# Kernel optimization log

Hardware: AMD Instinct MI355X
Metric: run time of the kernel (lower is better)

Reference implementation:

```python
import math
import jax, jax.numpy as jnp
import numpy as np

B, T, C = 4, 2048, 1024
NH, HD = 16, C // 16
FF = 4096
EPS = 1e-5


def _layernorm(x, g, b):
    mu = jnp.mean(x, axis=-1, keepdims=True)
    var = jnp.mean(jnp.square(x - mu), axis=-1, keepdims=True)
    return (x - mu) * jax.lax.rsqrt(var + EPS) * g + b


def _new_gelu(x):
    c = math.sqrt(2.0 / math.pi)
    return 0.5 * x * (1.0 + jnp.tanh(c * (x + 0.044715 * x * x * x)))


def setup_inputs() -> dict:
    key = jax.random.key(0)
    ks = jax.random.split(key, 5)
    s = lambda fan_in: 1.0 / math.sqrt(fan_in)
    return {
        "x": jax.random.normal(ks[0], (B, T, C), jnp.float32),
        "ln1_g": jnp.ones((C,), jnp.float32),
        "ln1_b": jnp.zeros((C,), jnp.float32),
        "w_qkv": jax.random.normal(ks[1], (C, 3 * C), jnp.float32) * s(C),
        "b_qkv": jnp.zeros((3 * C,), jnp.float32),
        "w_attn_proj": jax.random.normal(ks[2], (C, C), jnp.float32) * s(C),
        "b_attn_proj": jnp.zeros((C,), jnp.float32),
        "ln2_g": jnp.ones((C,), jnp.float32),
        "ln2_b": jnp.zeros((C,), jnp.float32),
        "w_fc": jax.random.normal(ks[3], (C, FF), jnp.float32) * s(C),
        "b_fc": jnp.zeros((FF,), jnp.float32),
        "w_mlp_proj": jax.random.normal(ks[4], (FF, C), jnp.float32) * s(FF),
        "b_mlp_proj": jnp.zeros((C,), jnp.float32),
    }


def reference(x, ln1_g, ln1_b, w_qkv, b_qkv, w_attn_proj, b_attn_proj,
              ln2_g, ln2_b, w_fc, b_fc, w_mlp_proj, b_mlp_proj):
    # --- attention branch ---
    h = _layernorm(x, ln1_g, ln1_b)
    qkv = h @ w_qkv + b_qkv                      # [B,T,3C]
    q, k, v = jnp.split(qkv, 3, axis=-1)
    # [B,T,C] -> [B,NH,T,HD]
    to_heads = lambda t: t.reshape(B, T, NH, HD).transpose(0, 2, 1, 3)
    q, k, v = to_heads(q), to_heads(k), to_heads(v)
    scores = jnp.einsum("bhqd,bhkd->bhqk", q, k) / math.sqrt(HD)  # [B,NH,T,T]
    causal = jnp.tril(jnp.ones((T, T), bool))
    scores = jnp.where(causal, scores, -jnp.inf)
    probs = jax.nn.softmax(scores, axis=-1)
    attn = jnp.einsum("bhqk,bhkd->bhqd", probs, v)  # [B,NH,T,HD]
    attn = attn.transpose(0, 2, 1, 3).reshape(B, T, C)
    x = x + attn @ w_attn_proj + b_attn_proj
    # --- MLP branch ---
    h = _layernorm(x, ln2_g, ln2_b)
    h = _new_gelu(h @ w_fc + b_fc)
    x = x + h @ w_mlp_proj + b_mlp_proj
    return x
```

## Files before the change

kernel.cpp:

```cpp
#include <hip/hip_runtime.h>
#include <hip/hip_bf16.h>

typedef __bf16 bf16x8 __attribute__((ext_vector_type(8)));
typedef __bf16 bf16x4 __attribute__((ext_vector_type(4)));
typedef float f32x4 __attribute__((ext_vector_type(4)));

__device__ __forceinline__ void gload16(const __bf16* g, __bf16* l) {
    __builtin_amdgcn_global_load_lds((const __attribute__((address_space(1))) void*)g,
                                     (__attribute__((address_space(3))) void*)l, 16, 0, 0);
}

__device__ __forceinline__ float gelu_f(float v) {
    float z = 0.7978845608028654f * (v + 0.044715f * v * v * v);
    float e = __expf(2.f * z);
    return 0.5f * v * (2.f - 2.f / (e + 1.f));
}

__device__ __forceinline__ int xcd_swizzle(int flat, int nwg) {
    return (flat & 7) * (nwg >> 3) + (flat >> 3);
}

__global__ __launch_bounds__(256) void diag_kernel(float* out, int n, float v) {
    int i = blockIdx.x * 256 + threadIdx.x;
    if (i < n) out[i] = v;
}

__global__ __launch_bounds__(256) void cvtT_kernel(
    const float* __restrict__ in, __bf16* __restrict__ out, int K, int N)
{
    __shared__ __bf16 tile[32][33];
    int bx = blockIdx.x * 32, by = blockIdx.y * 32;
    int tx = threadIdx.x & 31, ty = threadIdx.x >> 5;
#pragma unroll
    for (int i = 0; i < 32; i += 8)
        tile[ty + i][tx] = (__bf16)in[(size_t)(by + ty + i) * N + bx + tx];
    __syncthreads();
#pragma unroll
    for (int i = 0; i < 32; i += 8)
        out[(size_t)(bx + ty + i) * K + by + tx] = tile[tx][ty + i];
}

__global__ __launch_bounds__(256) void ln_kernel(
    const float* __restrict__ x, const float* __restrict__ g,
    const float* __restrict__ bta, __bf16* __restrict__ out)
{
    const int row = blockIdx.x, t = threadIdx.x;
    const float* xr = x + (size_t)row * 1024;
    float4 xv = ((const float4*)xr)[t];
    float f[4] = {xv.x, xv.y, xv.z, xv.w};
    float s = f[0] + f[1] + f[2] + f[3];
    float ss = f[0]*f[0] + f[1]*f[1] + f[2]*f[2] + f[3]*f[3];
#pragma unroll
    for (int off = 32; off; off >>= 1) {
        s  += __shfl_xor(s, off, 64);
        ss += __shfl_xor(ss, off, 64);
    }
    __shared__ float red[8];
    int lane = t & 63, w = t >> 6;
    if (lane == 0) { red[w] = s; red[4 + w] = ss; }
    __syncthreads();
    s  = red[0] + red[1] + red[2] + red[3];
    ss = red[4] + red[5] + red[6] + red[7];
    float mu = s * (1.f / 1024.f);
    float var = ss * (1.f / 1024.f) - mu * mu;
    float rstd = rsqrtf(fmaxf(var, 0.f) + 1e-5f);
    float4 gv = ((const float4*)g)[t];
    float4 bv = ((const float4*)bta)[t];
    bf16x4 ov;
    ov[0] = (__bf16)((f[0] - mu) * rstd * gv.x + bv.x);
    ov[1] = (__bf16)((f[1] - mu) * rstd * gv.y + bv.y);
    ov[2] = (__bf16)((f[2] - mu) * rstd * gv.z + bv.z);
    ov[3] = (__bf16)((f[3] - mu) * rstd * gv.w + bv.w);
    ((bf16x4*)(out + (size_t)row * 1024))[t] = ov;
}

template <int EPI>
__global__ __launch_bounds__(512, 2) void gemm256_kernel(
    const __bf16* __restrict__ A, const __bf16* __restrict__ BT,
    const float* __restrict__ bias, void* __restrict__ Cp, int M, int N, int K)
{
    __shared__ __align__(16) __bf16 lA[2][256 * 64];
    __shared__ __align__(16) __bf16 lB[2][256 * 64];
    const int t = threadIdx.x;
    const int lane = t & 63, w = t >> 6;
    const int wm = w >> 2, wn = w & 3;
    const int q4 = lane >> 4, r16 = lane & 15;
    const int nwg = gridDim.x * gridDim.y;
    const int nf = xcd_swizzle(blockIdx.y * gridDim.x + blockIdx.x, nwg);
    const int bm = (nf / gridDim.x) * 256, bn = (nf % gridDim.x) * 256;

    const int srow = t & 255;
    const int skc  = t >> 8;
    const __bf16* gA = A  + (size_t)(bm + srow) * K + skc * 8;
    const __bf16* gB = BT + (size_t)(bn + srow) * K + skc * 8;
    const int dst = skc * 2048 + srow * 8;

    f32x4 acc[8][4];
    f32x4 zero4 = {0.f, 0.f, 0.f, 0.f};
#pragma unroll
    for (int mi = 0; mi < 8; ++mi)
#pragma unroll
        for (int ni = 0; ni < 4; ++ni) acc[mi][ni] = zero4;

#pragma unroll
    for (int j = 0; j < 4; ++j) gload16(gA + j * 16, &lA[0][dst + j * 4096]);
#pragma unroll
    for (int j = 0; j < 4; ++j) gload16(gB + j * 16, &lB[0][dst + j * 4096]);
#pragma unroll
    for (int j = 0; j < 4; ++j) gload16(gA + 64 + j * 16, &lA[1][dst + j * 4096]);
    asm volatile("s_waitcnt vmcnt(4)" ::: "memory");
    __builtin_amdgcn_s_barrier();

    const int nt = K / 64;
    for (int ti = 0; ti < nt; ++ti) {
        const int p = ti & 1;
        bf16x8 af[4][2], bfr[2][2];
#pragma unroll
        for (int q = 0; q < 4; ++q) {
            const int qm = q >> 1, qn = q & 1;
            if (qn == 0) {
#pragma unroll
                for (int mi = 0; mi < 4; ++mi)
#pragma unroll
                    for (int ks = 0; ks < 2; ++ks)
                        af[mi][ks] = *(const bf16x8*)&lA[p][(ks * 4 + q4) * 2048 +
                            (wm * 128 + qm * 64 + mi * 16 + r16) * 8];
            }
#pragma unroll
            for (int ni = 0; ni < 2; ++ni)
#pragma unroll
                for (int ks = 0; ks < 2; ++ks)
                    bfr[ni][ks] = *(const bf16x8*)&lB[p][(ks * 4 + q4) * 2048 +
                        (wn * 64 + qn * 32 + ni * 16 + r16) * 8];
            if (q == 0 && ti + 1 < nt) {
                gload16(gB + (ti + 1) * 64,      &lB[p ^ 1][dst]);
                gload16(gB + (ti + 1) * 64 + 16, &lB[p ^ 1][dst + 4096]);
            }
            if (q == 1 && ti + 1 < nt) {
                gload16(gB + (ti + 1) * 64 + 32, &lB[p ^ 1][dst + 8192]);
                gload16(gB + (ti + 1) * 64 + 48, &lB[p ^ 1][dst + 12288]);
            }
            if (q == 3) {
                if (ti + 2 < nt) {
#pragma unroll
                    for (int j = 0; j < 4; ++j)
                        gload16(gA + (ti + 2) * 64 + j * 16, &lA[p][dst + j * 4096]);
                    asm volatile("s_waitcnt vmcnt(4)" ::: "memory");
                } else {
                    asm volatile("s_waitcnt vmcnt(0)" ::: "memory");
                }
            }
            __builtin_amdgcn_s_barrier();
            asm volatile("s_waitcnt lgkmcnt(0)" ::: "memory");
            __builtin_amdgcn_sched_barrier(0);
            __builtin_amdgcn_s_setprio(1);
#pragma unroll
            for (int mi = 0; mi < 4; ++mi)
#pragma unroll
                for (int ni = 0; ni < 2; ++ni) {
                    f32x4 v = acc[qm * 4 + mi][qn * 2 + ni];
                    v = __builtin_amdgcn_mfma_f32_16x16x32_bf16(af[mi][0], bfr[ni][0], v, 0, 0, 0);
                    v = __builtin_amdgcn_mfma_f32_16x16x32_bf16(af[mi][1], bfr[ni][1], v, 0, 0, 0);
                    acc[qm * 4 + mi][qn * 2 + ni] = v;
                }
            __builtin_amdgcn_s_setprio(0);
            __builtin_amdgcn_sched_barrier(0);
            __builtin_amdgcn_s_barrier();
        }
    }

#pragma unroll
    for (int mi = 0; mi < 8; ++mi) {
#pragma unroll
        for (int ni = 0; ni < 4; ++ni) {
#pragma unroll
            for (int i = 0; i < 4; ++i) {
                int r = bm + wm * 128 + mi * 16 + q4 * 4 + i;
                int c = bn + wn * 64 + ni * 16 + r16;
                float v = acc[mi][ni][i] + bias[c];
                if (EPI == 2) v = gelu_f(v);
                ((__bf16*)Cp)[(size_t)r * N + c] = (__bf16)v;
            }
        }
    }
}

template <int EPI>
__global__ __launch_bounds__(512, 2) void gemm128x256_kernel(
    const __bf16* __restrict__ A, const __bf16* __restrict__ BT,
    const float* __restrict__ bias, const float* __restrict__ res,
    float* __restrict__ C, int M, int N, int K)
{
    __shared__ __align__(16) __bf16 lA[2][128 * 64];
    __shared__ __align__(16) __bf16 lB[2][256 * 64];
    const int t = threadIdx.x;
    const int lane = t & 63, w = t >> 6;
    const int wm = w >> 2, wn = w & 3;
    const int q4 = lane >> 4, r16 = lane & 15;
    const int nwg = gridDim.x * gridDim.y;
    const int nf = xcd_swizzle(blockIdx.y * gridDim.x + blockIdx.x, nwg);
    const int bm = (nf / gridDim.x) * 128, bn = (nf % gridDim.x) * 256;

    const int srA = t & 127, kqA = t >> 7;
    const __bf16* gA = A + (size_t)(bm + srA) * K + kqA * 8;
    const int dstA = kqA * 1024 + srA * 8;
    const int srB = t & 255, skB = t >> 8;
    const __bf16* gB = BT + (size_t)(bn + srB) * K + skB * 8;
    const int dstB = skB * 2048 + srB * 8;

    f32x4 acc[4][4];
    f32x4 zero4 = {0.f, 0.f, 0.f, 0.f};
#pragma unroll
    for (int mi = 0; mi < 4; ++mi)
#pragma unroll
        for (int ni = 0; ni < 4; ++ni) acc[mi][ni] = zero4;

#pragma unroll
    for (int j = 0; j < 2; ++j) gload16(gA + j * 32, &lA[0][dstA + j * 4096]);
#pragma unroll
    for (int j = 0; j < 4; ++j) gload16(gB + j * 16, &lB[0][dstB + j * 4096]);
#pragma unroll
    for (int j = 0; j < 2; ++j) gload16(gA + 64 + j * 32, &lA[1][dstA + j * 4096]);
    asm volatile("s_waitcnt vmcnt(2)" ::: "memory");
    __builtin_amdgcn_s_barrier();

    const int nt = K / 64;
    for (int ti = 0; ti < nt; ++ti) {
        const int p = ti & 1;
        bf16x8 af[4][2], bfr[2][2];
#pragma unroll
        for (int qn = 0; qn < 2; ++qn) {
            if (qn == 0) {
#pragma unroll
                for (int mi = 0; mi < 4; ++mi)
#pragma unroll
                    for (int ks = 0; ks < 2; ++ks)
                        af[mi][ks] = *(const bf16x8*)&lA[p][(ks * 4 + q4) * 1024 +
                            (wm * 64 + mi * 16 + r16) * 8];
            }
#pragma unroll
            for (int ni = 0; ni < 2; ++ni)
#pragma unroll
                for (int ks = 0; ks < 2; ++ks)
                    bfr[ni][ks] = *(const bf16x8*)&lB[p][(ks * 4 + q4) * 2048 +
                        (wn * 64 + qn * 32 + ni * 16 + r16) * 8];
            if (qn == 0 && ti + 1 < nt) {
                gload16(gB + (ti + 1) * 64,      &lB[p ^ 1][dstB]);
                gload16(gB + (ti + 1) * 64 + 16, &lB[p ^ 1][dstB + 4096]);
                gload16(gB + (ti + 1) * 64 + 32, &lB[p ^ 1][dstB + 8192]);
                gload16(gB + (ti + 1) * 64 + 48, &lB[p ^ 1][dstB + 12288]);
            }
            if (qn == 1) {
                if (ti + 2 < nt) {
#pragma unroll
                    for (int j = 0; j < 2; ++j)
                        gload16(gA + (ti + 2) * 64 + j * 32, &lA[p][dstA + j * 4096]);
                    asm volatile("s_waitcnt vmcnt(2)" ::: "memory");
                } else {
                    asm volatile("s_waitcnt vmcnt(0)" ::: "memory");
                }
            }
            __builtin_amdgcn_s_barrier();
            asm volatile("s_waitcnt lgkmcnt(0)" ::: "memory");
            __builtin_amdgcn_sched_barrier(0);
            __builtin_amdgcn_s_setprio(1);
#pragma unroll
            for (int mi = 0; mi < 4; ++mi)
#pragma unroll
                for (int ni = 0; ni < 2; ++ni) {
                    f32x4 v = acc[mi][qn * 2 + ni];
                    v = __builtin_amdgcn_mfma_f32_16x16x32_bf16(af[mi][0], bfr[ni][0], v, 0, 0, 0);
                    v = __builtin_amdgcn_mfma_f32_16x16x32_bf16(af[mi][1], bfr[ni][1], v, 0, 0, 0);
                    acc[mi][qn * 2 + ni] = v;
                }
            __builtin_amdgcn_s_setprio(0);
            __builtin_amdgcn_sched_barrier(0);
            __builtin_amdgcn_s_barrier();
        }
    }

#pragma unroll
    for (int mi = 0; mi < 4; ++mi) {
#pragma unroll
        for (int ni = 0; ni < 4; ++ni) {
#pragma unroll
            for (int i = 0; i < 4; ++i) {
                int r = bm + wm * 64 + mi * 16 + q4 * 4 + i;
                int c = bn + wn * 64 + ni * 16 + r16;
                float v = acc[mi][ni][i] + bias[c];
                if (EPI == 1) v += res[(size_t)r * N + c];
                C[(size_t)r * N + c] = v;
            }
        }
    }
}

__global__ __launch_bounds__(256, 4) void attn_kernel(
    const __bf16* __restrict__ qkv, __bf16* __restrict__ attnb)
{
    __shared__ __align__(16) __bf16 lK[8192];
    __shared__ __align__(16) __bf16 lV[8192];
    __shared__ __align__(16) __bf16 lP[4][512];

    const int t = threadIdx.x, lane = t & 63, w = t >> 6;
    const int q4 = lane >> 4, r16 = lane & 15;
    const int flat = blockIdx.y * 16 + blockIdx.x;
    const int u = flat & 255, slot = flat >> 8, v5 = u & 15;
    const int cpat = (slot == 0) ? 0 : (slot == 1) ? 15 : (slot == 2) ? 5 : 10;
    const int qt = v5 ^ cpat;
    const int bh = (u >> 4) | (slot << 4);
    const int b = bh >> 4, h = bh & 15;
    const int qb = qt * 128;
    const __bf16* Qb = qkv + (size_t)b * 2048 * 3072 + h * 64;
    const __bf16* Kb = Qb + 1024;
    const __bf16* Vb = Qb + 2048;

    bf16x8 qf[2][2];
#pragma unroll
    for (int p = 0; p < 2; ++p) {
        int qrow = qb + p * 64 + w * 16 + r16;
        qf[p][0] = *(const bf16x8*)(Qb + (size_t)qrow * 3072 + q4 * 8);
        qf[p][1] = *(const bf16x8*)(Qb + (size_t)qrow * 3072 + 32 + q4 * 8);
#pragma unroll
        for (int j = 0; j < 8; ++j) {
            qf[p][0][j] = (__bf16)((float)qf[p][0][j] * 0.125f);
            qf[p][1][j] = (__bf16)((float)qf[p][1][j] * 0.125f);
        }
    }

    f32x4 zero4 = {0.f, 0.f, 0.f, 0.f};
    f32x4 o[2][4];
    float rs[2][4];
#pragma unroll
    for (int p = 0; p < 2; ++p)
#pragma unroll
        for (int i = 0; i < 4; ++i) { o[p][i] = zero4; rs[p][i] = 0.f; }

    const int skey = t & 127;
    const int vkc = t >> 6, svd = t & 63;

    for (int kb = 0; kb < qb + 128; kb += 128) {
        __syncthreads();
#pragma unroll
        for (int c = 0; c < 4; ++c)
            gload16(Kb + (size_t)(kb + skey) * 3072 + (c * 2 + (t >> 7)) * 8,
                    &lK[c * 2048 + t * 8]);
#pragma unroll
        for (int c = 0; c < 4; ++c) {
            int kc = c * 4 + vkc;
            bf16x8 vt;
#pragma unroll
            for (int j = 0; j < 8; ++j)
                vt[j] = Vb[(size_t)(kb + kc * 8 + j) * 3072 + svd];
            *(bf16x8*)&lV[kc * 512 + svd * 8] = vt;
        }
        __syncthreads();

#pragma unroll
        for (int p = 0; p < 2; ++p) {
            const int row0 = qb + p * 64 + w * 16 + q4 * 4;
            const bool interior = (kb + 127) <= (qb + p * 64 + w * 16);

            f32x4 s[8];
#pragma unroll
            for (int kg = 0; kg < 8; ++kg) {
                bf16x8 kfA = *(const bf16x8*)&lK[q4 * 1024 + (kg * 16 + r16) * 8];
                bf16x8 kfB = *(const bf16x8*)&lK[(4 + q4) * 1024 + (kg * 16 + r16) * 8];
                s[kg] = __builtin_amdgcn_mfma_f32_16x16x32_bf16(qf[p][0], kfA, zero4, 0, 0, 0);
                s[kg] = __builtin_amdgcn_mfma_f32_16x16x32_bf16(qf[p][1], kfB, s[kg], 0, 0, 0);
            }

#pragma unroll
            for (int kg = 0; kg < 8; ++kg)
#pragma unroll
                for (int i = 0; i < 4; ++i) {
                    float e = __expf(fminf(s[kg][i], 75.f));
                    if (!interior && (kb + kg * 16 + r16) > (row0 + i)) e = 0.f;
                    s[kg][i] = e;
                    rs[p][i] += e;
                }

#pragma unroll
            for (int c = 0; c < 4; ++c) {
#pragma unroll
                for (int kh = 0; kh < 2; ++kh)
#pragma unroll
                    for (int i = 0; i < 4; ++i)
                        lP[w][(kh * 2 + (r16 >> 3)) * 128 + (q4 * 4 + i) * 8 + (r16 & 7)] =
                            (__bf16)s[c * 2 + kh][i];
                asm volatile("s_waitcnt lgkmcnt(0)" ::: "memory");
                bf16x8 pf = *(const bf16x8*)&lP[w][q4 * 128 + r16 * 8];
#pragma unroll
                for (int ci = 0; ci < 4; ++ci) {
                    bf16x8 vf = *(const bf16x8*)&lV[(c * 4 + q4) * 512 + (ci * 16 + r16) * 8];
                    o[p][ci] = __builtin_amdgcn_mfma_f32_16x16x32_bf16(pf, vf, o[p][ci], 0, 0, 0);
                }
            }
        }
    }

#pragma unroll
    for (int p = 0; p < 2; ++p) {
#pragma unroll
        for (int off = 8; off; off >>= 1)
#pragma unroll
            for (int i = 0; i < 4; ++i) rs[p][i] += __shfl_xor(rs[p][i], off, 64);
#pragma unroll
        for (int ci = 0; ci < 4; ++ci)
#pragma unroll
            for (int i = 0; i < 4; ++i) {
                int trow = qb + p * 64 + w * 16 + q4 * 4 + i;
                float inv_l = (rs[p][i] > 0.f) ? (1.f / rs[p][i]) : 0.f;
                attnb[(size_t)(b * 2048 + trow) * 1024 + h * 64 + ci * 16 + r16] =
                    (__bf16)(o[p][ci][i] * inv_l);
            }
    }
}

extern "C" void kernel_launch(void* const* d_in, const int* in_sizes, int n_in,
                              void* d_out, int out_size, void* d_ws, size_t ws_size,
                              hipStream_t stream)
{
    const float* x      = (const float*)d_in[0];
    const float* ln1_g  = (const float*)d_in[1];
    const float* ln1_b  = (const float*)d_in[2];
    const float* w_qkv  = (const float*)d_in[3];
    const float* b_qkv  = (const float*)d_in[4];
    const float* w_proj = (const float*)d_in[5];
    const float* b_proj = (const float*)d_in[6];
    const float* ln2_g  = (const float*)d_in[7];
    const float* ln2_b  = (const float*)d_in[8];
    const float* w_fc   = (const float*)d_in[9];
    const float* b_fc   = (const float*)d_in[10];
    const float* w_mlp  = (const float*)d_in[11];
    const float* b_mlp  = (const float*)d_in[12];
    float* out = (float*)d_out;

    const size_t MiB = (size_t)1 << 20;
    if (ws_size < 136 * MiB) {
        float v = 1000.f + (float)(ws_size >> 20);
        diag_kernel<<<(out_size + 255) / 256, 256, 0, stream>>>(out, out_size, v);
        return;
    }

    char* ws = (char*)d_ws;
    __bf16* bufA   = (__bf16*)(ws);
    __bf16* bufB   = (__bf16*)(ws + 16 * MiB);
    float*  x1     = (float*) (ws + 80 * MiB);
    __bf16* wqkvT  = (__bf16*)(ws + 112 * MiB);
    __bf16* wprojT = (__bf16*)(ws + 118 * MiB);
    __bf16* wfcT   = (__bf16*)(ws + 120 * MiB);
    __bf16* wmlpT  = (__bf16*)(ws + 128 * MiB);

    cvtT_kernel<<<dim3(96, 32),  256, 0, stream>>>(w_qkv,  wqkvT,  1024, 3072);
    cvtT_kernel<<<dim3(32, 32),  256, 0, stream>>>(w_proj, wprojT, 1024, 1024);
    cvtT_kernel<<<dim3(128, 32), 256, 0, stream>>>(w_fc,   wfcT,   1024, 4096);
    cvtT_kernel<<<dim3(32, 128), 256, 0, stream>>>(w_mlp,  wmlpT,  4096, 1024);

    ln_kernel<<<8192, 256, 0, stream>>>(x, ln1_g, ln1_b, bufA);
    gemm256_kernel<0><<<dim3(12, 32), 512, 0, stream>>>(
        bufA, wqkvT, b_qkv, bufB, 8192, 3072, 1024);
    attn_kernel<<<dim3(16, 64), 256, 0, stream>>>(bufB, bufA);
    gemm128x256_kernel<1><<<dim3(4, 64), 512, 0, stream>>>(
        bufA, wprojT, b_proj, x, x1, 8192, 1024, 1024);
    ln_kernel<<<8192, 256, 0, stream>>>(x1, ln2_g, ln2_b, bufA);
    gemm256_kernel<2><<<dim3(16, 32), 512, 0, stream>>>(
        bufA, wfcT, b_fc, bufB, 8192, 4096, 1024);
    gemm128x256_kernel<1><<<dim3(4, 64), 512, 0, stream>>>(
        bufB, wmlpT, b_mlp, x1, out, 8192, 1024, 4096);
}
```

Measured before the change: 652.1 us.

## Skip masked causal key groups, double-buffer P tiles, use smaller GEMM tile for QKV

In the attention kernel, each wave computes how many 16-key groups intersect its causal region. It skips QK MFMAs, exp work and PV MFMAs for fully masked groups. The P staging buffer is doubled so the next P chunk can be written to LDS while the current one feeds MFMAs, which removes a serial store-wait-load step. The QKV projection moves from the 256-row GEMM to the 128x256 GEMM, which gains a bf16 output mode, giving 768 workgroups instead of 384 for better CU balance. Risks are extra branching and divergence inside the unrolled loops, and more LDS use that could lower occupancy.

After: 657.4 us. No clear change (+0.8%).

```diff
diff --git a/kernel.cpp b/kernel.cpp
--- a/kernel.cpp
+++ b/kernel.cpp
@@ -185,11 +185,11 @@
     }
 }
 
-template <int EPI>
+template <int EPI, bool OUT32>
 __global__ __launch_bounds__(512, 2) void gemm128x256_kernel(
     const __bf16* __restrict__ A, const __bf16* __restrict__ BT,
     const float* __restrict__ bias, const float* __restrict__ res,
-    float* __restrict__ C, int M, int N, int K)
+    void* __restrict__ Cp, int M, int N, int K)
 {
     __shared__ __align__(16) __bf16 lA[2][128 * 64];
     __shared__ __align__(16) __bf16 lB[2][256 * 64];
@@ -289,7 +289,8 @@
                 int c = bn + wn * 64 + ni * 16 + r16;
                 float v = acc[mi][ni][i] + bias[c];
                 if (EPI == 1) v += res[(size_t)r * N + c];
-                C[(size_t)r * N + c] = v;
+                if (OUT32) ((float*)Cp)[(size_t)r * N + c] = v;
+                else       ((__bf16*)Cp)[(size_t)r * N + c] = (__bf16)v;
             }
         }
     }
@@ -300,7 +301,7 @@
 {
     __shared__ __align__(16) __bf16 lK[8192];
     __shared__ __align__(16) __bf16 lV[8192];
-    __shared__ __align__(16) __bf16 lP[4][512];
+    __shared__ __align__(16) __bf16 lP[4][1024];
 
     const int t = threadIdx.x, lane = t & 63, w = t >> 6;
     const int q4 = lane >> 4, r16 = lane & 15;
@@ -360,40 +361,55 @@
         for (int p = 0; p < 2; ++p) {
             const int row0 = qb + p * 64 + w * 16 + q4 * 4;
             const bool interior = (kb + 127) <= (qb + p * 64 + w * 16);
+            int kgmax = ((qb + p * 64 + w * 16 + 15 - kb) >> 4) + 1;
+            kgmax = kgmax > 8 ? 8 : kgmax;
 
             f32x4 s[8];
 #pragma unroll
             for (int kg = 0; kg < 8; ++kg) {
-                bf16x8 kfA = *(const bf16x8*)&lK[q4 * 1024 + (kg * 16 + r16) * 8];
-                bf16x8 kfB = *(const bf16x8*)&lK[(4 + q4) * 1024 + (kg * 16 + r16) * 8];
-                s[kg] = __builtin_amdgcn_mfma_f32_16x16x32_bf16(qf[p][0], kfA, zero4, 0, 0, 0);
-                s[kg] = __builtin_amdgcn_mfma_f32_16x16x32_bf16(qf[p][1], kfB, s[kg], 0, 0, 0);
+                if (kg < kgmax) {
+                    bf16x8 kfA = *(const bf16x8*)&lK[q4 * 1024 + (kg * 16 + r16) * 8];
+                    bf16x8 kfB = *(const bf16x8*)&lK[(4 + q4) * 1024 + (kg * 16 + r16) * 8];
+                    s[kg] = __builtin_amdgcn_mfma_f32_16x16x32_bf16(qf[p][0], kfA, zero4, 0, 0, 0);
+                    s[kg] = __builtin_amdgcn_mfma_f32_16x16x32_bf16(qf[p][1], kfB, s[kg], 0, 0, 0);
+                } else {
+                    s[kg] = zero4;
+                }
             }
 
 #pragma unroll
             for (int kg = 0; kg < 8; ++kg)
-#pragma unroll
-                for (int i = 0; i < 4; ++i) {
-                    float e = __expf(fminf(s[kg][i], 75.f));
-                    if (!interior && (kb + kg * 16 + r16) > (row0 + i)) e = 0.f;
-                    s[kg][i] = e;
-                    rs[p][i] += e;
-                }
-
+                if (kg < kgmax)
+#pragma unroll
+                    for (int i = 0; i < 4; ++i) {
+                        float e = __expf(fminf(s[kg][i], 75.f));
+                        if (!interior && (kb + kg * 16 + r16) > (row0 + i)) e = 0.f;
+                        s[kg][i] = e;
+                        rs[p][i] += e;
+                    }
+
+            const int cmax = (kgmax + 1) >> 1;
+            auto storeP = [&](int c, int half) {
+#pragma unroll
+                for (int kh = 0; kh < 2; ++kh)
+#pragma unroll
+                    for (int i = 0; i < 4; ++i)
+                        lP[w][half * 512 + (kh * 2 + (r16 >> 3)) * 128 +
+                              (q4 * 4 + i) * 8 + (r16 & 7)] = (__bf16)s[c * 2 + kh][i];
+            };
+            storeP(0, 0);
 #pragma unroll
             for (int c = 0; c < 4; ++c) {
-#pragma unroll
-                for (int kh = 0; kh < 2; ++kh)
-#pragma unroll
-                    for (int i = 0; i < 4; ++i)
-                        lP[w][(kh * 2 + (r16 >> 3)) * 128 + (q4 * 4 + i) * 8 + (r16 & 7)] =
-                            (__bf16)s[c * 2 + kh][i];
-                asm volatile("s_waitcnt lgkmcnt(0)" ::: "memory");
-                bf16x8 pf = *(const bf16x8*)&lP[w][q4 * 128 + r16 * 8];
-#pragma unroll
-                for (int ci = 0; ci < 4; ++ci) {
-                    bf16x8 vf = *(const bf16x8*)&lV[(c * 4 + q4) * 512 + (ci * 16 + r16) * 8];
-                    o[p][ci] = __builtin_amdgcn_mfma_f32_16x16x32_bf16(pf, vf, o[p][ci], 0, 0, 0);
+                if (c < cmax) {
+                    asm volatile("s_waitcnt lgkmcnt(0)" ::: "memory");
+                    __builtin_amdgcn_sched_barrier(0);
+                    bf16x8 pf = *(const bf16x8*)&lP[w][(c & 1) * 512 + q4 * 128 + r16 * 8];
+                    if (c + 1 < cmax) storeP(c + 1, (c + 1) & 1);
+#pragma unroll
+                    for (int ci = 0; ci < 4; ++ci) {
+                        bf16x8 vf = *(const bf16x8*)&lV[(c * 4 + q4) * 512 + (ci * 16 + r16) * 8];
+                        o[p][ci] = __builtin_amdgcn_mfma_f32_16x16x32_bf16(pf, vf, o[p][ci], 0, 0, 0);
+                    }
                 }
             }
         }
@@ -458,14 +474,14 @@
     cvtT_kernel<<<dim3(32, 128), 256, 0, stream>>>(w_mlp,  wmlpT,  4096, 1024);
 
     ln_kernel<<<8192, 256, 0, stream>>>(x, ln1_g, ln1_b, bufA);
-    gemm256_kernel<0><<<dim3(12, 32), 512, 0, stream>>>(
-        bufA, wqkvT, b_qkv, bufB, 8192, 3072, 1024);
+    gemm128x256_kernel<0, false><<<dim3(12, 64), 512, 0, stream>>>(
+        bufA, wqkvT, b_qkv, nullptr, bufB, 8192, 3072, 1024);
     attn_kernel<<<dim3(16, 64), 256, 0, stream>>>(bufB, bufA);
-    gemm128x256_kernel<1><<<dim3(4, 64), 512, 0, stream>>>(
+    gemm128x256_kernel<1, true><<<dim3(4, 64), 512, 0, stream>>>(
         bufA, wprojT, b_proj, x, x1, 8192, 1024, 1024);
     ln_kernel<<<8192, 256, 0, stream>>>(x1, ln2_g, ln2_b, bufA);
     gemm256_kernel<2><<<dim3(16, 32), 512, 0, stream>>>(
         bufA, wfcT, b_fc, bufB, 8192, 4096, 1024);
-    gemm128x256_kernel<1><<<dim3(4, 64), 512, 0, stream>>>(
+    gemm128x256_kernel<1, true><<<dim3(4, 64), 512, 0, stream>>>(
         bufB, wmlpT, b_mlp, x1, out, 8192, 1024, 4096);
 }
```

## Triple-buffer B tiles in 128x256 GEMM and use it for QKV

Applied to the files above, without the earlier changes.

The 128x256 GEMM now keeps three LDS buffers for the B operand, so the B tile is prefetched two k-steps ahead instead of one. The vmcnt waits are adjusted to match the deeper queue. The kernel gains a bf16 output mode, and the QKV projection switches from the 256x256-tile kernel to this kernel with a grid of 768 workgroups. The deeper prefetch is meant to hide more global-load latency, and the smaller QKV tiles are meant to fill the CUs more evenly. The cost is more LDS per block and less operand reuse per tile for QKV.

Result: no change. 655.8 us (+0.6%).

```diff
diff --git a/kernel.cpp b/kernel.cpp
--- a/kernel.cpp
+++ b/kernel.cpp
@@ -185,14 +185,14 @@
     }
 }
 
-template <int EPI>
+template <int EPI, bool OUT32>
 __global__ __launch_bounds__(512, 2) void gemm128x256_kernel(
     const __bf16* __restrict__ A, const __bf16* __restrict__ BT,
     const float* __restrict__ bias, const float* __restrict__ res,
-    float* __restrict__ C, int M, int N, int K)
+    void* __restrict__ Cp, int M, int N, int K)
 {
     __shared__ __align__(16) __bf16 lA[2][128 * 64];
-    __shared__ __align__(16) __bf16 lB[2][256 * 64];
+    __shared__ __align__(16) __bf16 lB[3][256 * 64];
     const int t = threadIdx.x;
     const int lane = t & 63, w = t >> 6;
     const int wm = w >> 2, wn = w & 3;
@@ -221,12 +221,15 @@
     for (int j = 0; j < 4; ++j) gload16(gB + j * 16, &lB[0][dstB + j * 4096]);
 #pragma unroll
     for (int j = 0; j < 2; ++j) gload16(gA + 64 + j * 32, &lA[1][dstA + j * 4096]);
-    asm volatile("s_waitcnt vmcnt(2)" ::: "memory");
+#pragma unroll
+    for (int j = 0; j < 4; ++j) gload16(gB + 64 + j * 16, &lB[1][dstB + j * 4096]);
+    asm volatile("s_waitcnt vmcnt(6)" ::: "memory");
     __builtin_amdgcn_s_barrier();
 
     const int nt = K / 64;
+    int b0 = 0;
     for (int ti = 0; ti < nt; ++ti) {
-        const int p = ti & 1;
+        const int pa = ti & 1;
         bf16x8 af[4][2], bfr[2][2];
 #pragma unroll
         for (int qn = 0; qn < 2; ++qn) {
@@ -235,27 +238,28 @@
                 for (int mi = 0; mi < 4; ++mi)
 #pragma unroll
                     for (int ks = 0; ks < 2; ++ks)
-                        af[mi][ks] = *(const bf16x8*)&lA[p][(ks * 4 + q4) * 1024 +
+                        af[mi][ks] = *(const bf16x8*)&lA[pa][(ks * 4 + q4) * 1024 +
                             (wm * 64 + mi * 16 + r16) * 8];
             }
 #pragma unroll
             for (int ni = 0; ni < 2; ++ni)
 #pragma unroll
                 for (int ks = 0; ks < 2; ++ks)
-                    bfr[ni][ks] = *(const bf16x8*)&lB[p][(ks * 4 + q4) * 2048 +
+                    bfr[ni][ks] = *(const bf16x8*)&lB[b0][(ks * 4 + q4) * 2048 +
                         (wn * 64 + qn * 32 + ni * 16 + r16) * 8];
-            if (qn == 0 && ti + 1 < nt) {
-                gload16(gB + (ti + 1) * 64,      &lB[p ^ 1][dstB]);
-                gload16(gB + (ti + 1) * 64 + 16, &lB[p ^ 1][dstB + 4096]);
-                gload16(gB + (ti + 1) * 64 + 32, &lB[p ^ 1][dstB + 8192]);
-                gload16(gB + (ti + 1) * 64 + 48, &lB[p ^ 1][dstB + 12288]);
+            if (qn == 0 && ti + 2 < nt) {
+                int bs = b0 + 2; if (bs >= 3) bs -= 3;
+                gload16(gB + (ti + 2) * 64,      &lB[bs][dstB]);
+                gload16(gB + (ti + 2) * 64 + 16, &lB[bs][dstB + 4096]);
+                gload16(gB + (ti + 2) * 64 + 32, &lB[bs][dstB + 8192]);
+                gload16(gB + (ti + 2) * 64 + 48, &lB[bs][dstB + 12288]);
             }
             if (qn == 1) {
                 if (ti + 2 < nt) {
 #pragma unroll
                     for (int j = 0; j < 2; ++j)
-                        gload16(gA + (ti + 2) * 64 + j * 32, &lA[p][dstA + j * 4096]);
-                    asm volatile("s_waitcnt vmcnt(2)" ::: "memory");
+                        gload16(gA + (ti + 2) * 64 + j * 32, &lA[pa][dstA + j * 4096]);
+                    asm volatile("s_waitcnt vmcnt(6)" ::: "memory");
                 } else {
                     asm volatile("s_waitcnt vmcnt(0)" ::: "memory");
                 }
@@ -277,6 +281,7 @@
             __builtin_amdgcn_sched_barrier(0);
             __builtin_amdgcn_s_barrier();
         }
+        b0 = (b0 == 2) ? 0 : b0 + 1;
     }
 
 #pragma unroll
@@ -289,7 +294,8 @@
                 int c = bn + wn * 64 + ni * 16 + r16;
                 float v = acc[mi][ni][i] + bias[c];
                 if (EPI == 1) v += res[(size_t)r * N + c];
-                C[(size_t)r * N + c] = v;
+                if (OUT32) ((float*)Cp)[(size_t)r * N + c] = v;
+                else       ((__bf16*)Cp)[(size_t)r * N + c] = (__bf16)v;
             }
         }
     }
@@ -458,14 +464,14 @@
     cvtT_kernel<<<dim3(32, 128), 256, 0, stream>>>(w_mlp,  wmlpT,  4096, 1024);
 
     ln_kernel<<<8192, 256, 0, stream>>>(x, ln1_g, ln1_b, bufA);
-    gemm256_kernel<0><<<dim3(12, 32), 512, 0, stream>>>(
-        bufA, wqkvT, b_qkv, bufB, 8192, 3072, 1024);
+    gemm128x256_kernel<0, false><<<dim3(12, 64), 512, 0, stream>>>(
+        bufA, wqkvT, b_qkv, nullptr, bufB, 8192, 3072, 1024);
     attn_kernel<<<dim3(16, 64), 256, 0, stream>>>(bufB, bufA);
-    gemm128x256_kernel<1><<<dim3(4, 64), 512, 0, stream>>>(
+    gemm128x256_kernel<1, true><<<dim3(4, 64), 512, 0, stream>>>(
         bufA, wprojT, b_proj, x, x1, 8192, 1024, 1024);
     ln_kernel<<<8192, 256, 0, stream>>>(x1, ln2_g, ln2_b, bufA);
     gemm256_kernel<2><<<dim3(16, 32), 512, 0, stream>>>(
         bufA, wfcT, b_fc, bufB, 8192, 4096, 1024);
-    gemm128x256_kernel<1><<<dim3(4, 64), 512, 0, stream>>>(
+    gemm128x256_kernel<1, true><<<dim3(4, 64), 512, 0, stream>>>(
         bufB, wmlpT, b_mlp, x1, out, 8192, 1024, 4096);
 }
```
